# Kernel optimization log

Measured on AMD Instinct MI355X. Metric: run time of the kernel, lower is better.

Reference implementation:

```python
import jax, jax.numpy as jnp
import numpy as np
from math import sqrt

SIZE = 4096
NR_CORES = 2
RANK = 16
D = 64  # core_size: D**NR_CORES == SIZE


def setup_inputs() -> dict:
    key = jax.random.key(0)
    k_x, k_c0, k_c1, k_b = jax.random.split(key, 4)
    t = 1.0 / sqrt(SIZE)
    sigma = (t * sqrt(RANK) ** (1 - NR_CORES)) ** (1.0 / NR_CORES)
    x = jax.random.normal(k_x, (2, 4096, SIZE), dtype=jnp.float32)
    core0 = sigma * jax.random.normal(k_c0, (D, D, D, RANK, 1), dtype=jnp.float32)
    core1 = sigma * jax.random.normal(k_c1, (D, D, D, 1, RANK), dtype=jnp.float32)
    bias = sqrt(1.0 / SIZE) * jax.random.uniform(k_b, (SIZE,), minval=-1.0, maxval=1.0, dtype=jnp.float32)
    return {"x": x, "core0": core0, "core1": core1, "bias": bias}


def _btt_forward(x, cores, bias):
    d, c, size = D, NR_CORES, SIZE
    G = cores[0]  # (d,...,d, r, 1)
    for idx, core in enumerate(cores[1:]):
        j = d ** (idx + 1)
        i = d ** (c - idx - 1)
        core_r = core.reshape(j, d, i, core.shape[-2], core.shape[-1])
        G_r = G.reshape(j, d ** (idx + 1), i, G.shape[-2], G.shape[-1])
        # contract rank dim b: (j,x,i,cb) x (j,y,i,ba) -> (j,x,y,i,c,a)
        G = jnp.einsum('jxicb,jyiba->jxyica', core_r, G_r)
    G = G.reshape(size, size)
    out = x.reshape(-1, size) @ G + bias
    return out.reshape(x.shape)


def reference(x, core0, core1, bias):
    return _btt_forward(x, [core0, core1], bias)
```

## Files before the change

### kernel.cpp

```cpp
#include <hip/hip_runtime.h>
#include <hip/hip_bf16.h>
#include <stdint.h>
#include <stddef.h>

using bf16 = __hip_bfloat16;

typedef __attribute__((ext_vector_type(4))) float f32x4;
typedef __attribute__((ext_vector_type(8))) short bf16x8;
typedef __attribute__((ext_vector_type(4))) unsigned short u16x4;

#define K_DIM 4096
#define M_ROWS 8192
#define BM 256
#define BN 256
#define BK 64
#define NT (K_DIM / BK)
#define MT2 (M_ROWS / BM)
#define NT2 (K_DIM / BN)

template<int M> struct MC { static constexpr int value = M; };

__global__ void conv_bf16(const float* __restrict__ in, bf16* __restrict__ outb, int n4) {
  int idx = blockIdx.x * blockDim.x + threadIdx.x;
  int stride = gridDim.x * blockDim.x;
  for (int k = idx; k < n4; k += stride) {
    f32x4 v = ((const f32x4*)in)[k];
    bf16 tmp[4];
    tmp[0] = __float2bfloat16(v.x);
    tmp[1] = __float2bfloat16(v.y);
    tmp[2] = __float2bfloat16(v.z);
    tmp[3] = __float2bfloat16(v.w);
    ((u16x4*)outb)[k] = *(const u16x4*)tmp;
  }
}

__global__ void build_gt(const float* __restrict__ core0, const float* __restrict__ core1,
                         bf16* __restrict__ GT) {
  int j = blockIdx.x >> 6;
  int i = blockIdx.x & 63;
  __shared__ float c0s[64][16];
  __shared__ float c1s[64][16];
  int t = threadIdx.x;
#pragma unroll
  for (int rep = 0; rep < 4; ++rep) {
    int idx = rep * 256 + t;
    int row = idx >> 4;
    int b = idx & 15;
    size_t base = ((size_t)(j * 64 + row) * 64 + i) * 16 + b;
    c1s[row][b] = core1[base];
    c0s[row][b] = core0[base];
  }
  __syncthreads();
  int x = t & 63;
  int ys = t >> 6;
  float r1[16];
#pragma unroll
  for (int b = 0; b < 16; ++b) r1[b] = c1s[x][b];
#pragma unroll
  for (int yy = 0; yy < 16; ++yy) {
    int y = ys * 16 + yy;
    float acc = 0.f;
#pragma unroll
    for (int b = 0; b < 16; ++b) acc += r1[b] * c0s[y][b];
    GT[((size_t)(y * 64 + i) << 12) + (size_t)(j * 64 + x)] = __float2bfloat16(acc);
  }
}

__device__ __forceinline__ void gload_lds16(const bf16* g, bf16* l) {
  __builtin_amdgcn_global_load_lds(
      (const __attribute__((address_space(1))) unsigned int*)(g),
      (__attribute__((address_space(3))) unsigned int*)(l),
      16, 0, 0);
}

template<int MH>
__device__ __forceinline__ void read_a(bf16x8 (&af)[4][2], const bf16* As,
                                       int abase, int swk0, int swk1) {
#pragma unroll
  for (int mi = 0; mi < 4; ++mi) {
    int off = abase + (MH * 4 + mi) * 1024;
    af[mi][0] = *(const bf16x8*)&As[off + swk0];
    af[mi][1] = *(const bf16x8*)&As[off + swk1];
  }
}

template<int NH>
__device__ __forceinline__ void read_b(bf16x8 (&bfr)[4][2], const bf16* Bs,
                                       int bbase, int swk0, int swk1) {
#pragma unroll
  for (int ni = 0; ni < 2; ++ni) {
    int off = bbase + (NH * 2 + ni) * 1024;
    bfr[NH * 2 + ni][0] = *(const bf16x8*)&Bs[off + swk0];
    bfr[NH * 2 + ni][1] = *(const bf16x8*)&Bs[off + swk1];
  }
}

template<int MH, int NH>
__device__ __forceinline__ void mfma_quad(f32x4 (&acc)[8][4], const bf16x8 (&af)[4][2],
                                          const bf16x8 (&bfr)[4][2]) {
#pragma unroll
  for (int mi = 0; mi < 4; ++mi)
#pragma unroll
    for (int ni = 0; ni < 2; ++ni)
#pragma unroll
      for (int kk = 0; kk < 2; ++kk)
        acc[MH * 4 + mi][NH * 2 + ni] = __builtin_amdgcn_mfma_f32_16x16x32_bf16(
            af[mi][kk], bfr[NH * 2 + ni][kk], acc[MH * 4 + mi][NH * 2 + ni], 0, 0, 0);
}

#define BARRIER() asm volatile("s_barrier" ::: "memory")
#define SP1() __builtin_amdgcn_s_setprio(1)
#define SP0() __builtin_amdgcn_s_setprio(0)
#define VMCNT8() asm volatile("s_waitcnt vmcnt(8)" ::: "memory")
#define VMCNT4() asm volatile("s_waitcnt vmcnt(4)" ::: "memory")
#define VMCNT0() asm volatile("s_waitcnt vmcnt(0)" ::: "memory")
#define LGKM0()  asm volatile("s_waitcnt lgkmcnt(0)" ::: "memory")

__global__ __launch_bounds__(512, 2)
void gemm_xg(const bf16* __restrict__ Xb, const bf16* __restrict__ GT,
             const float* __restrict__ bias, float* __restrict__ out) {
  __shared__ bf16 As[2][BM * BK];
  __shared__ bf16 Bs[2][BN * BK];

  int bid = blockIdx.x;
  int sb = (bid & 7) * (MT2 * NT2 / 8) + (bid >> 3);
  int bm = sb >> 4;
  int bn = sb & 15;

  int t = threadIdx.x;
  int lane = t & 63;
  int wid = t >> 6;

  int srow = t >> 3;
  int scol = t & 7;
  int sxor = scol ^ (srow & 7);
  const bf16* gA0 = Xb + ((size_t)(bm * BM + srow) * K_DIM) + sxor * 8;
  const bf16* gB0 = GT + ((size_t)(bn * BN + srow) * K_DIM) + sxor * 8;
  int lbase = srow * BK + scol * 8;

  auto sA = [&](int buf, int h, int kt) {
    const bf16* g = gA0 + (size_t)(h * 128) * K_DIM + (size_t)kt * BK;
    bf16* l = &As[buf][h * 128 * BK + lbase];
    gload_lds16(g, l);
    gload_lds16(g + (size_t)64 * K_DIM, l + 64 * BK);
  };
  auto sB = [&](int buf, int h, int kt) {
    const bf16* g = gB0 + (size_t)(h * 128) * K_DIM + (size_t)kt * BK;
    bf16* l = &Bs[buf][h * 128 * BK + lbase];
    gload_lds16(g, l);
    gload_lds16(g + (size_t)64 * K_DIM, l + 64 * BK);
  };

  int wm = wid >> 2;
  int wn = wid & 3;
  int lr = lane & 15;
  int g4 = lane >> 4;
  int x7 = lr & 7;
  int swk0 = ((g4 ^ x7) << 3);
  int swk1 = (((4 + g4) ^ x7) << 3);
  int abase = (wm * 128 + lr) * BK;
  int bbase = (wn * 64 + lr) * BK;

  f32x4 acc[8][4] = {};
  bf16x8 af[4][2];
  bf16x8 bfr[4][2];

  const bf16* Ab[2] = { &As[0][0], &As[1][0] };
  const bf16* Bb[2] = { &Bs[0][0], &Bs[1][0] };

  sB(0, 0, 0); sB(0, 1, 0);
  sA(0, 0, 0); sA(0, 1, 0);
  sB(1, 0, 1); sB(1, 1, 1);
  sA(1, 0, 1); sA(1, 1, 1);
  VMCNT8();
  BARRIER();
  read_a<0>(af, Ab[0], abase, swk0, swk1);
  read_b<0>(bfr, Bb[0], bbase, swk0, swk1);
  read_b<1>(bfr, Bb[0], bbase, swk0, swk1);
  LGKM0();
  BARRIER();

  auto tile = [&](int kt, int CUR, auto modec) {
    constexpr int MODE = decltype(modec)::value;
    const int OTH = CUR ^ 1;
    const bf16* Ac = Ab[CUR];
    const bf16* Ao = Ab[OTH];
    const bf16* Bo = Bb[OTH];

    SP1(); mfma_quad<0, 0>(acc, af, bfr); SP0();
    if (MODE == 0) sB(CUR, 0, kt + 2);
    SP1(); mfma_quad<0, 1>(acc, af, bfr); SP0();
    read_a<1>(af, Ac, abase, swk0, swk1);
    if (MODE == 0) sB(CUR, 1, kt + 2);
    LGKM0();
    if (MODE == 0) { VMCNT4(); } else { VMCNT0(); }
    BARRIER();

    SP1(); mfma_quad<1, 0>(acc, af, bfr); SP0();
    if (MODE < 2) read_b<0>(bfr, Bo, bbase, swk0, swk1);
    if (MODE == 0) sA(CUR, 0, kt + 2);
    SP1(); mfma_quad<1, 1>(acc, af, bfr); SP0();
    if (MODE < 2) {
      read_b<1>(bfr, Bo, bbase, swk0, swk1);
      read_a<0>(af, Ao, abase, swk0, swk1);
    }
    if (MODE == 0) sA(CUR, 1, kt + 2);
    LGKM0();
    BARRIER();
  };

#pragma unroll 1
  for (int i = 0; i < NT / 2 - 1; ++i) {
    tile(2 * i,     0, MC<0>{});
    tile(2 * i + 1, 1, MC<0>{});
  }
  tile(NT - 2, 0, MC<1>{});
  tile(NT - 1, 1, MC<2>{});

  int colbase = bn * BN + wn * 64 + lr;
  int rowbase = bm * BM + wm * 128 + g4 * 4;
#pragma unroll
  for (int ni = 0; ni < 4; ++ni) {
    int col = colbase + ni * 16;
    float bv = bias[col];
#pragma unroll
    for (int mi = 0; mi < 8; ++mi) {
#pragma unroll
      for (int r = 0; r < 4; ++r) {
        int row = rowbase + mi * 16 + r;
        out[(size_t)row * K_DIM + col] = acc[mi][ni][r] + bv;
      }
    }
  }
}

extern "C" void kernel_launch(void* const* d_in, const int* in_sizes, int n_in,
                              void* d_out, int out_size, void* d_ws, size_t ws_size,
                              hipStream_t stream) {
  const float* x     = (const float*)d_in[0];
  const float* core0 = (const float*)d_in[1];
  const float* core1 = (const float*)d_in[2];
  const float* bias  = (const float*)d_in[3];
  float* out = (float*)d_out;

  bf16* Xb = (bf16*)d_ws;
  bf16* GT = (bf16*)((char*)d_ws + (size_t)M_ROWS * K_DIM * sizeof(bf16));

  conv_bf16<<<2048, 256, 0, stream>>>(x, Xb, (M_ROWS * K_DIM) / 4);
  build_gt<<<4096, 256, 0, stream>>>(core0, core1, GT);
  gemm_xg<<<MT2 * NT2, 512, 0, stream>>>(Xb, GT, bias, out);
}
```

Measured before the change: 295.4 us.

## Restructure GEMM main loop pipeline with staggered A/B prefetch distances

Reworks the software pipeline of the bf16 GEMM main loop. A tiles are now prefetched one K-tile ahead and B tiles two ahead, and LDS fragment reads are placed just before each MFMA quad with a barrier between quads, replacing the old scheme that read the next tile's fragments during the current tile's MFMAs. The MFMA loop order is also changed so the kk dimension is outermost, which puts independent accumulators back to back. The intent is to spread global-to-LDS traffic more evenly and reduce stalls, at the cost of more barriers per tile and less overlap between LDS reads and MFMAs.

```diff
diff --git a/kernel.cpp b/kernel.cpp
--- a/kernel.cpp
+++ b/kernel.cpp
@@ -99,22 +99,21 @@
 __device__ __forceinline__ void mfma_quad(f32x4 (&acc)[8][4], const bf16x8 (&af)[4][2],
                                           const bf16x8 (&bfr)[4][2]) {
 #pragma unroll
-  for (int mi = 0; mi < 4; ++mi)
-#pragma unroll
-    for (int ni = 0; ni < 2; ++ni)
-#pragma unroll
-      for (int kk = 0; kk < 2; ++kk)
+  for (int kk = 0; kk < 2; ++kk)
+#pragma unroll
+    for (int mi = 0; mi < 4; ++mi)
+#pragma unroll
+      for (int ni = 0; ni < 2; ++ni)
         acc[MH * 4 + mi][NH * 2 + ni] = __builtin_amdgcn_mfma_f32_16x16x32_bf16(
             af[mi][kk], bfr[NH * 2 + ni][kk], acc[MH * 4 + mi][NH * 2 + ni], 0, 0, 0);
 }
 
 #define BARRIER() asm volatile("s_barrier" ::: "memory")
+#define LGKM0() asm volatile("s_waitcnt lgkmcnt(0)" ::: "memory")
 #define SP1() __builtin_amdgcn_s_setprio(1)
 #define SP0() __builtin_amdgcn_s_setprio(0)
-#define VMCNT8() asm volatile("s_waitcnt vmcnt(8)" ::: "memory")
 #define VMCNT4() asm volatile("s_waitcnt vmcnt(4)" ::: "memory")
 #define VMCNT0() asm volatile("s_waitcnt vmcnt(0)" ::: "memory")
-#define LGKM0()  asm volatile("s_waitcnt lgkmcnt(0)" ::: "memory")
 
 __global__ __launch_bounds__(512, 2)
 void gemm_xg(const bf16* __restrict__ Xb, const bf16* __restrict__ GT,
@@ -168,46 +167,41 @@
   const bf16* Ab[2] = { &As[0][0], &As[1][0] };
   const bf16* Bb[2] = { &Bs[0][0], &Bs[1][0] };
 
+  auto tile = [&](int kt, int cur, auto modec) {
+    constexpr int MODE = decltype(modec)::value;
+    const bf16* Ac = Ab[cur];
+    const bf16* Bc = Bb[cur];
+    const int nb = cur ^ 1;
+
+    if (MODE == 2) { VMCNT0(); } else { VMCNT4(); }
+    read_a<0>(af, Ac, abase, swk0, swk1);
+    read_b<0>(bfr, Bc, bbase, swk0, swk1);
+    if (MODE < 2) sA(nb, 0, kt + 1);
+    LGKM0();
+    BARRIER();
+    SP1(); mfma_quad<0, 0>(acc, af, bfr); SP0();
+
+    read_b<1>(bfr, Bc, bbase, swk0, swk1);
+    if (MODE < 2) sA(nb, 1, kt + 1);
+    LGKM0();
+    BARRIER();
+    SP1(); mfma_quad<0, 1>(acc, af, bfr); SP0();
+
+    read_a<1>(af, Ac, abase, swk0, swk1);
+    if (MODE == 0) sB(cur, 0, kt + 2);
+    LGKM0();
+    BARRIER();
+    SP1(); mfma_quad<1, 0>(acc, af, bfr); SP0();
+
+    if (MODE == 0) sB(cur, 1, kt + 2);
+    SP1(); mfma_quad<1, 1>(acc, af, bfr); SP0();
+  };
+
   sB(0, 0, 0); sB(0, 1, 0);
   sA(0, 0, 0); sA(0, 1, 0);
   sB(1, 0, 1); sB(1, 1, 1);
-  sA(1, 0, 1); sA(1, 1, 1);
-  VMCNT8();
+  VMCNT4();
   BARRIER();
-  read_a<0>(af, Ab[0], abase, swk0, swk1);
-  read_b<0>(bfr, Bb[0], bbase, swk0, swk1);
-  read_b<1>(bfr, Bb[0], bbase, swk0, swk1);
-  LGKM0();
-  BARRIER();
-
-  auto tile = [&](int kt, int CUR, auto modec) {
-    constexpr int MODE = decltype(modec)::value;
-    const int OTH = CUR ^ 1;
-    const bf16* Ac = Ab[CUR];
-    const bf16* Ao = Ab[OTH];
-    const bf16* Bo = Bb[OTH];
-
-    SP1(); mfma_quad<0, 0>(acc, af, bfr); SP0();
-    if (MODE == 0) sB(CUR, 0, kt + 2);
-    SP1(); mfma_quad<0, 1>(acc, af, bfr); SP0();
-    read_a<1>(af, Ac, abase, swk0, swk1);
-    if (MODE == 0) sB(CUR, 1, kt + 2);
-    LGKM0();
-    if (MODE == 0) { VMCNT4(); } else { VMCNT0(); }
-    BARRIER();
-
-    SP1(); mfma_quad<1, 0>(acc, af, bfr); SP0();
-    if (MODE < 2) read_b<0>(bfr, Bo, bbase, swk0, swk1);
-    if (MODE == 0) sA(CUR, 0, kt + 2);
-    SP1(); mfma_quad<1, 1>(acc, af, bfr); SP0();
-    if (MODE < 2) {
-      read_b<1>(bfr, Bo, bbase, swk0, swk1);
-      read_a<0>(af, Ao, abase, swk0, swk1);
-    }
-    if (MODE == 0) sA(CUR, 1, kt + 2);
-    LGKM0();
-    BARRIER();
-  };
 
 #pragma unroll 1
   for (int i = 0; i < NT / 2 - 1; ++i) {
```

New measurement: 285.5 us, median of 3. 3.3% less time.
